# Kernel tuning notes

Measured on AMD Instinct MI355X. Metric: run time of the kernel, lower is better.

Reference implementation:

```python
import jax, jax.numpy as jnp
import numpy as np

Q_HEADS, KV_HEADS, DIMS = 16, 4, 1024
HEAD_DIM = DIMS // Q_HEADS          # 64
GROUPS = Q_HEADS // KV_HEADS        # 4
ROPE_BASE = 10000.0


def rope(x):
    # x: (..., s, d) -- standard interleaved rotary embedding, base 10000
    s, d = x.shape[-2], x.shape[-1]
    inv_freq = 1.0 / (ROPE_BASE ** (jnp.arange(0, d, 2, dtype=jnp.float32) / d))
    ang = jnp.arange(s, dtype=jnp.float32)[:, None] * inv_freq[None, :]  # (s, d/2)
    cos, sin = jnp.cos(ang), jnp.sin(ang)
    x1, x2 = x[..., 0::2], x[..., 1::2]
    out = jnp.stack([x1 * cos - x2 * sin, x1 * sin + x2 * cos], axis=-1)
    return out.reshape(x.shape).astype(x.dtype)


def setup_inputs() -> dict:
    key = jax.random.key(0)
    k1, k2, k3, k4, k5, k6 = jax.random.split(key, 6)
    B, S, E = 4, 2048, 1024
    q = jax.random.normal(k1, (B, S, E), dtype=jnp.float32)
    kv = jax.random.normal(k2, (B, S, E), dtype=jnp.float32)
    sc = 1.0 / np.sqrt(E)
    Wq = jax.random.normal(k3, (E, Q_HEADS, HEAD_DIM), dtype=jnp.float32) * sc
    Wk = jax.random.normal(k4, (E, KV_HEADS, HEAD_DIM), dtype=jnp.float32) * sc
    Wv = jax.random.normal(k5, (E, KV_HEADS, HEAD_DIM), dtype=jnp.float32) * sc
    Wo = jax.random.normal(k6, (HEAD_DIM, E), dtype=jnp.float32) / np.sqrt(HEAD_DIM)
    return {"q": q, "kv": kv, "Wq": Wq, "Wk": Wk, "Wv": Wv, "Wo": Wo}


def reference(q, kv, Wq, Wk, Wv, Wo):
    B, S, E = q.shape
    qh = jnp.einsum('bse,ehd->bshd', q, Wq)    # (B,S,Q_HEADS,hd)
    kh = jnp.einsum('bse,ehd->bshd', kv, Wk)   # (B,S,KV_HEADS,hd)
    vh = jnp.einsum('bse,ehd->bshd', kv, Wv)
    # rearrange '... s (h g) d -> ... g h s d' with g=GROUPS (h = KV_HEADS outer)
    qh = qh.reshape(B, S, KV_HEADS, GROUPS, HEAD_DIM).transpose(0, 3, 2, 1, 4)  # (B,g,h,S,d)
    kh = kh.transpose(0, 2, 1, 3)  # (B,h,S,d)
    vh = vh.transpose(0, 2, 1, 3)  # (B,h,S,d)
    qh = rope(qh)
    kh = rope(kh)
    # NOTE: sums over group axis g (faithful to original einsum)
    scores = jnp.einsum('bghsd,bhad->bhsa', qh, kh)
    attn = jax.nn.softmax(scores / (HEAD_DIM ** 0.5), axis=-1)
    out = jnp.einsum('bhsa,bhad->bhsd', attn, vh)  # (B,h,S,d)
    out = out.mean(axis=1)                          # mean over kv heads -> (B,S,d)
    return out @ Wo                                 # (B,S,E)
```

## Files before the change

### kernel.cpp

```cpp
#include <hip/hip_runtime.h>
#include <math.h>

#define SS 2048
#define EE 1024

using bf16x8 = __attribute__((ext_vector_type(8))) short;
using f32x4  = __attribute__((ext_vector_type(4))) float;

__device__ inline short f2bf(float x) {
    unsigned u = __builtin_bit_cast(unsigned, x);
    return (short)((u + 0x7fffu + ((u >> 16) & 1u)) >> 16);
}
__device__ inline short f2bf_r(float x) {
    return (short)((__builtin_bit_cast(unsigned, x) + 0x8000u) >> 16);
}
__device__ inline unsigned pk_bf16(float a, float b) {
    unsigned ua = __builtin_bit_cast(unsigned, a) + 0x8000u;
    unsigned ub = __builtin_bit_cast(unsigned, b) + 0x8000u;
    return __builtin_amdgcn_perm(ub, ua, 0x07060302u);
}

__global__ __launch_bounds__(256) void prep_weights(const float* __restrict__ Wq,
                                                    const float* __restrict__ Wk,
                                                    const float* __restrict__ Wv,
                                                    const float* __restrict__ Wo,
                                                    short* __restrict__ Wall,
                                                    short* __restrict__ Wo4,
                                                    float2* __restrict__ RT) {
    int idx = blockIdx.x * 256 + threadIdx.x;
    int c = idx >> 10, e = idx & 1023;
    int h = c >> 6, d = c & 63;
    const float* p = Wq + (size_t)e * 1024 + h * 256 + d;
    Wall[(size_t)c * 1024 + e] = f2bf(0.18033688011112042f * (p[0] + p[64] + p[128] + p[192]));
    Wall[(size_t)(256 + c) * 1024 + e] = f2bf(Wk[(size_t)e * 256 + c]);
    Wall[(size_t)(512 + c) * 1024 + e] = f2bf(Wv[(size_t)e * 256 + c]);
    Wo4[(size_t)e * 256 + c] = f2bf(0.25f * Wo[(size_t)d * 1024 + e]);
    if (idx < 65536) {
        int s = idx >> 5, ii = idx & 31;
        float freq = __expf(-(float)ii * (9.210340371976184f / 32.0f));
        float sn, cs;
        sincosf((float)s * freq, &sn, &cs);
        RT[idx] = (float2){cs, sn};
    }
}

__global__ __launch_bounds__(256) void proj_kernel(const float* __restrict__ q,
                                                   const float* __restrict__ kv,
                                                   const short* __restrict__ Wall,
                                                   const float2* __restrict__ RT,
                                                   short* __restrict__ Qb,
                                                   short* __restrict__ Kb,
                                                   short* __restrict__ Vt) {
    __shared__ alignas(16) short As[128][72];
    __shared__ alignas(16) short Bs[64][72];
    int tid = threadIdx.x;
    int wave = tid >> 6, lane = tid & 63, quad = lane >> 4, c16 = lane & 15;
    int wm = wave >> 1, wn = wave & 1;
    int m0 = blockIdx.x * 128, n0 = blockIdx.y * 64;
    const float* A = (n0 < 256) ? q : kv;

    f32x4 acc[4][2];
    #pragma unroll
    for (int i = 0; i < 4; i++)
        #pragma unroll
        for (int j = 0; j < 2; j++) acc[i][j] = (f32x4){0.f, 0.f, 0.f, 0.f};

    for (int k0 = 0; k0 < 1024; k0 += 64) {
        #pragma unroll
        for (int i = 0; i < 8; i++) {
            int id = i * 256 + tid, r = id >> 4, ch = id & 15;
            float4 v = *(const float4*)&A[(size_t)(m0 + r) * 1024 + k0 + ch * 4];
            uint2 u;
            u.x = pk_bf16(v.x, v.y);
            u.y = pk_bf16(v.z, v.w);
            *(uint2*)&As[r][ch * 4] = u;
        }
        #pragma unroll
        for (int i = 0; i < 2; i++) {
            int id = i * 256 + tid, r = id >> 3, ch = id & 7;
            *(int4*)&Bs[r][ch * 8] =
                *(const int4*)&Wall[(size_t)(n0 + r) * 1024 + k0 + ch * 8];
        }
        __syncthreads();
        #pragma unroll
        for (int ks = 0; ks < 64; ks += 32) {
            bf16x8 af[4], bfr[2];
            #pragma unroll
            for (int mt = 0; mt < 4; mt++)
                af[mt] = *(const bf16x8*)&As[wm * 64 + mt * 16 + c16][ks + quad * 8];
            #pragma unroll
            for (int nt = 0; nt < 2; nt++)
                bfr[nt] = *(const bf16x8*)&Bs[wn * 32 + nt * 16 + c16][ks + quad * 8];
            #pragma unroll
            for (int mt = 0; mt < 4; mt++)
                #pragma unroll
                for (int nt = 0; nt < 2; nt++)
                    acc[mt][nt] = __builtin_amdgcn_mfma_f32_16x16x32_bf16(
                        af[mt], bfr[nt], acc[mt][nt], 0, 0, 0);
        }
        __syncthreads();
    }
    if (n0 < 512) {
        #pragma unroll
        for (int mt = 0; mt < 4; mt++) {
            #pragma unroll
            for (int nt = 0; nt < 2; nt++) {
                int cl = wn * 32 + nt * 16 + c16;
                int ii = ((n0 + cl) & 63) >> 1;
                float sgn = (lane & 1) ? 1.0f : -1.0f;
                f32x4 v = acc[mt][nt];
                #pragma unroll
                for (int r = 0; r < 4; r++) {
                    int rl = wm * 64 + mt * 16 + quad * 4 + r;
                    float2 cs = RT[((m0 + rl) & (SS - 1)) * 32 + ii];
                    float other = __shfl_xor(v[r], 1);
                    As[rl][cl] = f2bf_r(v[r] * cs.x + sgn * cs.y * other);
                }
            }
        }
        __syncthreads();
        short* dstb = (n0 < 256) ? Qb : Kb;
        int nc0 = n0 & 255;
        #pragma unroll
        for (int i = 0; i < 4; i++) {
            int id = i * 256 + tid, r = id >> 3, ch = id & 7;
            *(int4*)&dstb[(size_t)(m0 + r) * 256 + nc0 + ch * 8] =
                *(const int4*)&As[r][ch * 8];
        }
    } else {
        short (*Lt)[136] = (short(*)[136])&As[0][0];
        #pragma unroll
        for (int mt = 0; mt < 4; mt++) {
            #pragma unroll
            for (int nt = 0; nt < 2; nt++) {
                int cl = wn * 32 + nt * 16 + c16;
                int sl = wm * 64 + mt * 16 + quad * 4;
                f32x4 v = acc[mt][nt];
                uint2 u;
                u.x = pk_bf16(v[0], v[1]);
                u.y = pk_bf16(v[2], v[3]);
                *(uint2*)&Lt[cl][sl] = u;
            }
        }
        __syncthreads();
        int b = m0 >> 11, s0 = m0 & (SS - 1), c0 = n0 - 512;
        #pragma unroll
        for (int i = 0; i < 4; i++) {
            int id = i * 256 + tid, c = id >> 4, ch = id & 15;
            *(int4*)&Vt[((size_t)(b * 256 + c0 + c)) * SS + s0 + ch * 8] =
                *(const int4*)&Lt[c][ch * 8];
        }
    }
}

__global__ __launch_bounds__(256, 5) void attn_kernel(const short* __restrict__ Qb,
                                                      const short* __restrict__ Kb,
                                                      const short* __restrict__ Vt,
                                                      float* __restrict__ Opart,
                                                      float* __restrict__ Lpart) {
    __shared__ alignas(16) short Qs[64][72];
    __shared__ alignas(16) short Ks[64][72], Vs[64][72];
    int tid = threadIdx.x;
    int wave = tid >> 6, lane = tid & 63, quad = lane >> 4, c16 = lane & 15;
    int qt = blockIdx.x, bh = blockIdx.y, kc = blockIdx.z;
    int q0 = qt * 64;
    size_t qkbase = (size_t)(bh >> 2) * SS * 256 + (bh & 3) * 64;
    size_t vtbase = (size_t)(bh * 64) * SS;
    size_t pbase  = (size_t)(kc * 16 + bh) * SS;

    #pragma unroll
    for (int i = 0; i < 2; i++) {
        int id = i * 256 + tid, r = id >> 3, ch = id & 7;
        *(int4*)&Qs[r][ch * 8] = *(const int4*)&Qb[qkbase + (size_t)(q0 + r) * 256 + ch * 8];
    }
    __syncthreads();
    bf16x8 aq0 = *(const bf16x8*)&Qs[wave * 16 + c16][quad * 8];
    bf16x8 aq1 = *(const bf16x8*)&Qs[wave * 16 + c16][32 + quad * 8];
    short (*Ps)[72] = (short (*)[72])Qs[wave * 16];

    float lsum[4] = {0.f, 0.f, 0.f, 0.f};
    f32x4 o[4];
    #pragma unroll
    for (int dt = 0; dt < 4; dt++) o[dt] = (f32x4){0.f, 0.f, 0.f, 0.f};

    for (int kt = 0; kt < 16; kt++) {
        int a0 = kc * 1024 + kt * 64;
        __syncthreads();
        #pragma unroll
        for (int i = 0; i < 2; i++) {
            int id = i * 256 + tid, r = id >> 3, ch = id & 7;
            *(int4*)&Ks[r][ch * 8] =
                *(const int4*)&Kb[qkbase + (size_t)(a0 + r) * 256 + ch * 8];
            *(int4*)&Vs[r][ch * 8] =
                *(const int4*)&Vt[vtbase + (size_t)r * SS + a0 + ch * 8];
        }
        __syncthreads();
        f32x4 sv[4];
        #pragma unroll
        for (int nt = 0; nt < 4; nt++) sv[nt] = (f32x4){0.f, 0.f, 0.f, 0.f};
        #pragma unroll
        for (int nt = 0; nt < 4; nt++) {
            bf16x8 bk0 = *(const bf16x8*)&Ks[nt * 16 + c16][quad * 8];
            bf16x8 bk1 = *(const bf16x8*)&Ks[nt * 16 + c16][32 + quad * 8];
            sv[nt] = __builtin_amdgcn_mfma_f32_16x16x32_bf16(aq0, bk0, sv[nt], 0, 0, 0);
            sv[nt] = __builtin_amdgcn_mfma_f32_16x16x32_bf16(aq1, bk1, sv[nt], 0, 0, 0);
        }
        #pragma unroll
        for (int nt = 0; nt < 4; nt++)
            #pragma unroll
            for (int r = 0; r < 4; r++) sv[nt][r] = __builtin_exp2f(sv[nt][r]);
        #pragma unroll
        for (int r = 0; r < 4; r++)
            lsum[r] += (sv[0][r] + sv[1][r]) + (sv[2][r] + sv[3][r]);
        #pragma unroll
        for (int nt = 0; nt < 4; nt++)
            #pragma unroll
            for (int r = 0; r < 4; r++)
                Ps[quad * 4 + r][nt * 16 + c16] = f2bf_r(sv[nt][r]);
        #pragma unroll
        for (int ks = 0; ks < 64; ks += 32) {
            bf16x8 ap = *(const bf16x8*)&Ps[c16][ks + quad * 8];
            #pragma unroll
            for (int dt = 0; dt < 4; dt++) {
                bf16x8 bv = *(const bf16x8*)&Vs[dt * 16 + c16][ks + quad * 8];
                o[dt] = __builtin_amdgcn_mfma_f32_16x16x32_bf16(ap, bv, o[dt], 0, 0, 0);
            }
        }
    }
    #pragma unroll
    for (int off = 1; off < 16; off <<= 1)
        #pragma unroll
        for (int r = 0; r < 4; r++) lsum[r] += __shfl_xor(lsum[r], off);
    #pragma unroll
    for (int dt = 0; dt < 4; dt++)
        #pragma unroll
        for (int r = 0; r < 4; r++) {
            int row = q0 + wave * 16 + quad * 4 + r;
            Opart[(pbase + row) * 64 + dt * 16 + c16] = o[dt][r];
        }
    if (c16 == 0)
        #pragma unroll
        for (int r = 0; r < 4; r++)
            Lpart[pbase + q0 + wave * 16 + quad * 4 + r] = lsum[r];
}

__global__ __launch_bounds__(256) void outproj_kernel(const float* __restrict__ Op,
                                                      const float* __restrict__ Lp,
                                                      const short* __restrict__ Wo4,
                                                      float* __restrict__ out) {
    __shared__ alignas(16) short As[64][72];
    __shared__ alignas(16) short Bs[128][72];
    int tid = threadIdx.x;
    int wave = tid >> 6, lane = tid & 63, quad = lane >> 4, c16 = lane & 15;
    int wm = wave >> 1, wn = wave & 1;
    int m0 = blockIdx.x * 64, n0 = blockIdx.y * 128;

    f32x4 acc[2][4];
    #pragma unroll
    for (int i = 0; i < 2; i++)
        #pragma unroll
        for (int j = 0; j < 4; j++) acc[i][j] = (f32x4){0.f, 0.f, 0.f, 0.f};

    for (int k0 = 0; k0 < 256; k0 += 64) {
        int h = k0 >> 6;
        #pragma unroll
        for (int i = 0; i < 4; i++) {
            int id = i * 256 + tid, r = id >> 4, ch = id & 15;
            int row = m0 + r, b = row >> 11, s = row & (SS - 1);
            int bh = b * 4 + h;
            size_t pidx = ((size_t)bh * SS + s) * 64 + ch * 4;
            float4 a = *(const float4*)&Op[pidx];
            float4 c = *(const float4*)&Op[pidx + (size_t)16 * SS * 64];
            float l = Lp[(size_t)bh * SS + s] + Lp[(size_t)(16 + bh) * SS + s];
            float rl = __builtin_amdgcn_rcpf(l);
            uint2 u;
            u.x = pk_bf16((a.x + c.x) * rl, (a.y + c.y) * rl);
            u.y = pk_bf16((a.z + c.z) * rl, (a.w + c.w) * rl);
            *(uint2*)&As[r][ch * 4] = u;
        }
        #pragma unroll
        for (int i = 0; i < 4; i++) {
            int id = i * 256 + tid, r = id >> 3, ch = id & 7;
            *(int4*)&Bs[r][ch * 8] =
                *(const int4*)&Wo4[(size_t)(n0 + r) * 256 + k0 + ch * 8];
        }
        __syncthreads();
        #pragma unroll
        for (int ks = 0; ks < 64; ks += 32) {
            bf16x8 af[2], bfr[4];
            #pragma unroll
            for (int mt = 0; mt < 2; mt++)
                af[mt] = *(const bf16x8*)&As[wm * 32 + mt * 16 + c16][ks + quad * 8];
            #pragma unroll
            for (int nt = 0; nt < 4; nt++)
                bfr[nt] = *(const bf16x8*)&Bs[wn * 64 + nt * 16 + c16][ks + quad * 8];
            #pragma unroll
            for (int mt = 0; mt < 2; mt++)
                #pragma unroll
                for (int nt = 0; nt < 4; nt++)
                    acc[mt][nt] = __builtin_amdgcn_mfma_f32_16x16x32_bf16(
                        af[mt], bfr[nt], acc[mt][nt], 0, 0, 0);
        }
        __syncthreads();
    }
    #pragma unroll
    for (int mt = 0; mt < 2; mt++)
        #pragma unroll
        for (int nt = 0; nt < 4; nt++) {
            int col = n0 + wn * 64 + nt * 16 + c16;
            int rowb = m0 + wm * 32 + mt * 16 + quad * 4;
            #pragma unroll
            for (int r = 0; r < 4; r++)
                out[(size_t)(rowb + r) * 1024 + col] = acc[mt][nt][r];
        }
}

extern "C" void kernel_launch(void* const* d_in, const int* in_sizes, int n_in,
                              void* d_out, int out_size, void* d_ws, size_t ws_size,
                              hipStream_t stream) {
    const float* q  = (const float*)d_in[0];
    const float* kv = (const float*)d_in[1];
    const float* Wq = (const float*)d_in[2];
    const float* Wk = (const float*)d_in[3];
    const float* Wv = (const float*)d_in[4];
    const float* Wo = (const float*)d_in[5];
    float* out = (float*)d_out;

    short* Qb    = (short*)d_ws;
    short* Kb    = Qb + 2097152;
    short* Vt    = Kb + 2097152;
    short* Wall  = Vt + 2097152;
    short* Wo4   = Wall + 786432;
    float2* RT   = (float2*)(Wo4 + 262144);
    float* Opart = (float*)(RT + 65536);
    float* Lpart = Opart + 4194304;

    prep_weights<<<1024, 256, 0, stream>>>(Wq, Wk, Wv, Wo, Wall, Wo4, RT);

    proj_kernel<<<dim3(64, 12), 256, 0, stream>>>(q, kv, Wall, RT, Qb, Kb, Vt);

    attn_kernel<<<dim3(32, 16, 2), 256, 0, stream>>>(Qb, Kb, Vt, Opart, Lpart);

    outproj_kernel<<<dim3(128, 8), 256, 0, stream>>>(Opart, Lpart, Wo4, out);
}
```

Measured before the change: 208.4 us.

## Merge split-K attention halves in-block and emit bf16 output for outproj

The attention kernel now uses 512-thread blocks in which two groups of four waves each process one half of the key range. The halves are combined in shared memory, normalized by the summed exp totals, and written as a bf16 (B,S,256) tensor. This removes the fp32 Opart/Lpart partial buffers and the reduce-and-convert step in outproj, which now loads bf16 directly and uses 128x128 tiles. The cost is half as many attention blocks, larger LDS use, and extra barriers in the epilogue.

```diff
diff --git a/kernel.cpp b/kernel.cpp
--- a/kernel.cpp
+++ b/kernel.cpp
@@ -153,55 +153,56 @@
     }
 }
 
-__global__ __launch_bounds__(256, 5) void attn_kernel(const short* __restrict__ Qb,
+__global__ __launch_bounds__(512, 4) void attn_kernel(const short* __restrict__ Qb,
                                                       const short* __restrict__ Kb,
                                                       const short* __restrict__ Vt,
-                                                      float* __restrict__ Opart,
-                                                      float* __restrict__ Lpart) {
+                                                      short* __restrict__ Ob) {
     __shared__ alignas(16) short Qs[64][72];
-    __shared__ alignas(16) short Ks[64][72], Vs[64][72];
+    __shared__ alignas(16) short Ps2[64][72];
+    __shared__ alignas(16) short Ks[2][64][72];
+    __shared__ alignas(16) short Vs[2][64][72];
     int tid = threadIdx.x;
     int wave = tid >> 6, lane = tid & 63, quad = lane >> 4, c16 = lane & 15;
-    int qt = blockIdx.x, bh = blockIdx.y, kc = blockIdx.z;
+    int rq = wave & 3, kh = wave >> 2;
+    int qt = blockIdx.x, bh = blockIdx.y;
     int q0 = qt * 64;
     size_t qkbase = (size_t)(bh >> 2) * SS * 256 + (bh & 3) * 64;
     size_t vtbase = (size_t)(bh * 64) * SS;
-    size_t pbase  = (size_t)(kc * 16 + bh) * SS;
-
-    #pragma unroll
-    for (int i = 0; i < 2; i++) {
-        int id = i * 256 + tid, r = id >> 3, ch = id & 7;
+
+    {
+        int r = tid >> 3, ch = tid & 7;
         *(int4*)&Qs[r][ch * 8] = *(const int4*)&Qb[qkbase + (size_t)(q0 + r) * 256 + ch * 8];
     }
     __syncthreads();
-    bf16x8 aq0 = *(const bf16x8*)&Qs[wave * 16 + c16][quad * 8];
-    bf16x8 aq1 = *(const bf16x8*)&Qs[wave * 16 + c16][32 + quad * 8];
-    short (*Ps)[72] = (short (*)[72])Qs[wave * 16];
+    bf16x8 aq0 = *(const bf16x8*)&Qs[rq * 16 + c16][quad * 8];
+    bf16x8 aq1 = *(const bf16x8*)&Qs[rq * 16 + c16][32 + quad * 8];
+    short (*Ps)[72] = (kh == 0) ? (short (*)[72])Qs[rq * 16] : (short (*)[72])Ps2[rq * 16];
 
     float lsum[4] = {0.f, 0.f, 0.f, 0.f};
     f32x4 o[4];
     #pragma unroll
     for (int dt = 0; dt < 4; dt++) o[dt] = (f32x4){0.f, 0.f, 0.f, 0.f};
 
+    int sr = tid >> 3, sch = tid & 7;
     for (int kt = 0; kt < 16; kt++) {
-        int a0 = kc * 1024 + kt * 64;
-        __syncthreads();
-        #pragma unroll
-        for (int i = 0; i < 2; i++) {
-            int id = i * 256 + tid, r = id >> 3, ch = id & 7;
-            *(int4*)&Ks[r][ch * 8] =
-                *(const int4*)&Kb[qkbase + (size_t)(a0 + r) * 256 + ch * 8];
-            *(int4*)&Vs[r][ch * 8] =
-                *(const int4*)&Vt[vtbase + (size_t)r * SS + a0 + ch * 8];
-        }
+        int a0 = kt * 64;
+        __syncthreads();
+        *(int4*)&Ks[0][sr][sch * 8] =
+            *(const int4*)&Kb[qkbase + (size_t)(a0 + sr) * 256 + sch * 8];
+        *(int4*)&Ks[1][sr][sch * 8] =
+            *(const int4*)&Kb[qkbase + (size_t)(1024 + a0 + sr) * 256 + sch * 8];
+        *(int4*)&Vs[0][sr][sch * 8] =
+            *(const int4*)&Vt[vtbase + (size_t)sr * SS + a0 + sch * 8];
+        *(int4*)&Vs[1][sr][sch * 8] =
+            *(const int4*)&Vt[vtbase + (size_t)sr * SS + 1024 + a0 + sch * 8];
         __syncthreads();
         f32x4 sv[4];
         #pragma unroll
         for (int nt = 0; nt < 4; nt++) sv[nt] = (f32x4){0.f, 0.f, 0.f, 0.f};
         #pragma unroll
         for (int nt = 0; nt < 4; nt++) {
-            bf16x8 bk0 = *(const bf16x8*)&Ks[nt * 16 + c16][quad * 8];
-            bf16x8 bk1 = *(const bf16x8*)&Ks[nt * 16 + c16][32 + quad * 8];
+            bf16x8 bk0 = *(const bf16x8*)&Ks[kh][nt * 16 + c16][quad * 8];
+            bf16x8 bk1 = *(const bf16x8*)&Ks[kh][nt * 16 + c16][32 + quad * 8];
             sv[nt] = __builtin_amdgcn_mfma_f32_16x16x32_bf16(aq0, bk0, sv[nt], 0, 0, 0);
             sv[nt] = __builtin_amdgcn_mfma_f32_16x16x32_bf16(aq1, bk1, sv[nt], 0, 0, 0);
         }
@@ -222,7 +223,7 @@
             bf16x8 ap = *(const bf16x8*)&Ps[c16][ks + quad * 8];
             #pragma unroll
             for (int dt = 0; dt < 4; dt++) {
-                bf16x8 bv = *(const bf16x8*)&Vs[dt * 16 + c16][ks + quad * 8];
+                bf16x8 bv = *(const bf16x8*)&Vs[kh][dt * 16 + c16][ks + quad * 8];
                 o[dt] = __builtin_amdgcn_mfma_f32_16x16x32_bf16(ap, bv, o[dt], 0, 0, 0);
             }
         }
@@ -231,71 +232,79 @@
     for (int off = 1; off < 16; off <<= 1)
         #pragma unroll
         for (int r = 0; r < 4; r++) lsum[r] += __shfl_xor(lsum[r], off);
-    #pragma unroll
-    for (int dt = 0; dt < 4; dt++)
+
+    __syncthreads();
+    float (*Ox)[68] = (float (*)[68])&Ks[0][0][0];
+    float* Lx = (float*)&Vs[0][0][0];
+    short (*Ot)[72] = (short (*)[72])&Vs[1][0][0];
+    int base = rq * 16 + quad * 4;
+    if (wave >= 4) {
+        #pragma unroll
+        for (int dt = 0; dt < 4; dt++)
+            #pragma unroll
+            for (int r = 0; r < 4; r++)
+                Ox[base + r][dt * 16 + c16] = o[dt][r];
+        if (c16 == 0)
+            #pragma unroll
+            for (int r = 0; r < 4; r++) Lx[base + r] = lsum[r];
+    }
+    __syncthreads();
+    if (wave < 4) {
         #pragma unroll
         for (int r = 0; r < 4; r++) {
-            int row = q0 + wave * 16 + quad * 4 + r;
-            Opart[(pbase + row) * 64 + dt * 16 + c16] = o[dt][r];
-        }
-    if (c16 == 0)
-        #pragma unroll
-        for (int r = 0; r < 4; r++)
-            Lpart[pbase + q0 + wave * 16 + quad * 4 + r] = lsum[r];
-}
-
-__global__ __launch_bounds__(256) void outproj_kernel(const float* __restrict__ Op,
-                                                      const float* __restrict__ Lp,
+            float rl = __builtin_amdgcn_rcpf(lsum[r] + Lx[base + r]);
+            #pragma unroll
+            for (int dt = 0; dt < 4; dt++)
+                Ot[base + r][dt * 16 + c16] =
+                    f2bf_r((o[dt][r] + Ox[base + r][dt * 16 + c16]) * rl);
+        }
+    }
+    __syncthreads();
+    {
+        int r = tid >> 3, ch = tid & 7;
+        int b = bh >> 2, h = bh & 3;
+        *(int4*)&Ob[((size_t)(b * SS + q0 + r)) * 256 + h * 64 + ch * 8] =
+            *(const int4*)&Ot[r][ch * 8];
+    }
+}
+
+__global__ __launch_bounds__(256) void outproj_kernel(const short* __restrict__ Ob,
                                                       const short* __restrict__ Wo4,
                                                       float* __restrict__ out) {
-    __shared__ alignas(16) short As[64][72];
+    __shared__ alignas(16) short As[128][72];
     __shared__ alignas(16) short Bs[128][72];
     int tid = threadIdx.x;
     int wave = tid >> 6, lane = tid & 63, quad = lane >> 4, c16 = lane & 15;
     int wm = wave >> 1, wn = wave & 1;
-    int m0 = blockIdx.x * 64, n0 = blockIdx.y * 128;
-
-    f32x4 acc[2][4];
-    #pragma unroll
-    for (int i = 0; i < 2; i++)
+    int m0 = blockIdx.x * 128, n0 = blockIdx.y * 128;
+
+    f32x4 acc[4][4];
+    #pragma unroll
+    for (int i = 0; i < 4; i++)
         #pragma unroll
         for (int j = 0; j < 4; j++) acc[i][j] = (f32x4){0.f, 0.f, 0.f, 0.f};
 
     for (int k0 = 0; k0 < 256; k0 += 64) {
-        int h = k0 >> 6;
-        #pragma unroll
-        for (int i = 0; i < 4; i++) {
-            int id = i * 256 + tid, r = id >> 4, ch = id & 15;
-            int row = m0 + r, b = row >> 11, s = row & (SS - 1);
-            int bh = b * 4 + h;
-            size_t pidx = ((size_t)bh * SS + s) * 64 + ch * 4;
-            float4 a = *(const float4*)&Op[pidx];
-            float4 c = *(const float4*)&Op[pidx + (size_t)16 * SS * 64];
-            float l = Lp[(size_t)bh * SS + s] + Lp[(size_t)(16 + bh) * SS + s];
-            float rl = __builtin_amdgcn_rcpf(l);
-            uint2 u;
-            u.x = pk_bf16((a.x + c.x) * rl, (a.y + c.y) * rl);
-            u.y = pk_bf16((a.z + c.z) * rl, (a.w + c.w) * rl);
-            *(uint2*)&As[r][ch * 4] = u;
-        }
         #pragma unroll
         for (int i = 0; i < 4; i++) {
             int id = i * 256 + tid, r = id >> 3, ch = id & 7;
+            *(int4*)&As[r][ch * 8] =
+                *(const int4*)&Ob[(size_t)(m0 + r) * 256 + k0 + ch * 8];
             *(int4*)&Bs[r][ch * 8] =
                 *(const int4*)&Wo4[(size_t)(n0 + r) * 256 + k0 + ch * 8];
         }
         __syncthreads();
         #pragma unroll
         for (int ks = 0; ks < 64; ks += 32) {
-            bf16x8 af[2], bfr[4];
-            #pragma unroll
-            for (int mt = 0; mt < 2; mt++)
-                af[mt] = *(const bf16x8*)&As[wm * 32 + mt * 16 + c16][ks + quad * 8];
+            bf16x8 af[4], bfr[4];
+            #pragma unroll
+            for (int mt = 0; mt < 4; mt++)
+                af[mt] = *(const bf16x8*)&As[wm * 64 + mt * 16 + c16][ks + quad * 8];
             #pragma unroll
             for (int nt = 0; nt < 4; nt++)
                 bfr[nt] = *(const bf16x8*)&Bs[wn * 64 + nt * 16 + c16][ks + quad * 8];
             #pragma unroll
-            for (int mt = 0; mt < 2; mt++)
+            for (int mt = 0; mt < 4; mt++)
                 #pragma unroll
                 for (int nt = 0; nt < 4; nt++)
                     acc[mt][nt] = __builtin_amdgcn_mfma_f32_16x16x32_bf16(
@@ -304,11 +313,11 @@
         __syncthreads();
     }
     #pragma unroll
-    for (int mt = 0; mt < 2; mt++)
+    for (int mt = 0; mt < 4; mt++)
         #pragma unroll
         for (int nt = 0; nt < 4; nt++) {
             int col = n0 + wn * 64 + nt * 16 + c16;
-            int rowb = m0 + wm * 32 + mt * 16 + quad * 4;
+            int rowb = m0 + wm * 64 + mt * 16 + quad * 4;
             #pragma unroll
             for (int r = 0; r < 4; r++)
                 out[(size_t)(rowb + r) * 1024 + col] = acc[mt][nt][r];
@@ -332,14 +341,13 @@
     short* Wall  = Vt + 2097152;
     short* Wo4   = Wall + 786432;
     float2* RT   = (float2*)(Wo4 + 262144);
-    float* Opart = (float*)(RT + 65536);
-    float* Lpart = Opart + 4194304;
+    short* Ob    = (short*)(RT + 65536);
 
     prep_weights<<<1024, 256, 0, stream>>>(Wq, Wk, Wv, Wo, Wall, Wo4, RT);
 
     proj_kernel<<<dim3(64, 12), 256, 0, stream>>>(q, kv, Wall, RT, Qb, Kb, Vt);
 
-    attn_kernel<<<dim3(32, 16, 2), 256, 0, stream>>>(Qb, Kb, Vt, Opart, Lpart);
-
-    outproj_kernel<<<dim3(128, 8), 256, 0, stream>>>(Opart, Lpart, Wo4, out);
-}
+    attn_kernel<<<dim3(32, 16), 512, 0, stream>>>(Qb, Kb, Vt, Ob);
+
+    outproj_kernel<<<dim3(64, 8), 256, 0, stream>>>(Ob, Wo4, out);
+}
```

Measured after the change: 207.8 us. About the same (-0.3%).
